# Optimization experiments

Hardware: AMD Instinct MI355X
Metric: run time of the kernel (lower is better)

Reference implementation:

```python
import jax, jax.numpy as jnp
import numpy as np
import math

NH = 12      # num attention heads
WIN = 128    # one-sided sliding window
NG = 32      # number of global (prefix) tokens
NEG = -1e9
LN_EPS = 1e-12


def _layernorm(x, g, b):
    mu = jnp.mean(x, axis=-1, keepdims=True)
    var = jnp.mean(jnp.square(x - mu), axis=-1, keepdims=True)
    return (x - mu) * jax.lax.rsqrt(var + LN_EPS) * g + b


def _longformer_self_attn(h, am, Wq, bq, Wk, bk, Wv, bv):
    B, S, D = h.shape
    Dh = D // NH
    w = WIN
    C = S // w  # number of chunks

    def proj(Wm, bm):
        return (h @ Wm + bm).reshape(B, S, NH, Dh).transpose(0, 2, 1, 3)

    q = proj(Wq, bq) * (1.0 / math.sqrt(Dh))  # [B,H,S,Dh]
    k = proj(Wk, bk)
    v = proj(Wv, bv)

    # ---- banded (sliding window) scores, chunked: each query chunk sees 3w keys ----
    kp = jnp.pad(k, ((0, 0), (0, 0), (w, w), (0, 0)))
    vp = jnp.pad(v, ((0, 0), (0, 0), (w, w), (0, 0)))
    idx = jnp.arange(C)[:, None] * w + jnp.arange(3 * w)[None, :]  # [C,3w]
    k3 = kp[:, :, idx]  # [B,H,C,3w,Dh]
    v3 = vp[:, :, idx]
    qc = q.reshape(B, NH, C, w, Dh)
    band = jnp.einsum('bhcqd,bhckd->bhcqk', qc, k3)  # [B,H,C,w,3w]

    qpos = (jnp.arange(C) * w)[:, None, None] + jnp.arange(w)[None, :, None]  # [C,w,1]
    kpos = (idx - w)[:, None, :]  # [C,1,3w] absolute key positions
    valid = (jnp.abs(kpos - qpos) <= w) & (kpos >= NG) & (kpos < S)  # band, exclude global keys

    amp = jnp.pad(am, ((0, 0), (w, w)))
    am3 = amp[:, idx]  # [B,C,3w] additive mask gathered per chunk
    band = band + am3[:, None, :, None, :]
    band = jnp.where(valid[None, None], band, NEG)
    band = band.reshape(B, NH, S, 3 * w)

    # ---- every token also attends to the NG global tokens ----
    gsc = jnp.einsum('bhsd,bhgd->bhsg', q, k[:, :, :NG]) + am[:, None, None, :NG]

    logits = jnp.concatenate([band, gsc], axis=-1)  # [B,H,S,3w+NG]
    probs = jax.nn.softmax(logits, axis=-1)
    pb = probs[..., :3 * w].reshape(B, NH, C, w, 3 * w)
    out = jnp.einsum('bhcqk,bhckd->bhcqd', pb, v3).reshape(B, NH, S, Dh)
    out = out + jnp.einsum('bhsg,bhgd->bhsd', probs[..., 3 * w:], v[:, :, :NG])

    # ---- global tokens attend to everything ----
    gl = jnp.einsum('bhgd,bhsd->bhgs', q[:, :, :NG], k) + am[:, None, None, :]
    outg = jnp.einsum('bhgs,bhsd->bhgd', jax.nn.softmax(gl, axis=-1), v)

    ctx = jnp.concatenate([outg, out[:, :, NG:]], axis=2)  # [B,H,S,Dh]
    return ctx.transpose(0, 2, 1, 3).reshape(B, S, D)


def setup_inputs() -> dict:
    key = jax.random.key(0)
    ks = jax.random.split(key, 8)
    B, S, D, F = 2, 4096, 768, 3072
    p = lambda k_, sh: jax.random.normal(k_, sh, jnp.float32) * 0.02
    return {
        'hidden_states': jax.random.normal(ks[0], (B, S, D), jnp.float32),
        'attention_mask': jnp.zeros((B, S), jnp.float32),
        'Wq': p(ks[1], (D, D)), 'bq': jnp.zeros((D,), jnp.float32),
        'Wk': p(ks[2], (D, D)), 'bk': jnp.zeros((D,), jnp.float32),
        'Wv': p(ks[3], (D, D)), 'bv': jnp.zeros((D,), jnp.float32),
        'Wo': p(ks[4], (D, D)), 'bo': jnp.zeros((D,), jnp.float32),
        'ln1_g': jnp.ones((D,), jnp.float32), 'ln1_b': jnp.zeros((D,), jnp.float32),
        'Wi': p(ks[5], (D, F)), 'bi': jnp.zeros((F,), jnp.float32),
        'Wo2': p(ks[6], (F, D)), 'bo2': jnp.zeros((D,), jnp.float32),
        'ln2_g': jnp.ones((D,), jnp.float32), 'ln2_b': jnp.zeros((D,), jnp.float32),
    }


def reference(hidden_states, attention_mask, Wq, bq, Wk, bk, Wv, bv, Wo, bo,
              ln1_g, ln1_b, Wi, bi, Wo2, bo2, ln2_g, ln2_b):
    ctx = _longformer_self_attn(hidden_states, attention_mask, Wq, bq, Wk, bk, Wv, bv)
    attn_out = _layernorm(ctx @ Wo + bo + hidden_states, ln1_g, ln1_b)
    inter = jax.nn.gelu(attn_out @ Wi + bi, approximate=False)
    layer_out = _layernorm(inter @ Wo2 + bo2 + attn_out, ln2_g, ln2_b)
    return layer_out
```

## Files before the change

kernel.cpp:

```cpp
#include <hip/hip_runtime.h>
#include <math.h>

#define NHEAD 12
#define DH 64
#define S_LEN 4096
#define B_SZ 2
#define D_MODEL 768
#define FF_DIM 3072
#define WINSZ 128
#define NGLB 32
#define NEGV -1e9f
#define NQC 6291456L

typedef __attribute__((ext_vector_type(8))) short bf16x8;
typedef __attribute__((ext_vector_type(4))) float floatx4;

__device__ __forceinline__ unsigned short f2bf(float x) {
    union { float f; unsigned u; } v; v.f = x;
    unsigned r = v.u + 0x7fffu + ((v.u >> 16) & 1u);
    return (unsigned short)(r >> 16);
}
__device__ __forceinline__ float bf2f(unsigned short x) {
    union { unsigned u; float f; } v; v.u = ((unsigned)x) << 16;
    return v.f;
}

__device__ __forceinline__ void async_copy16(const unsigned short* g, unsigned short* l) {
    __builtin_amdgcn_global_load_lds(
        (const __attribute__((address_space(1))) void*)g,
        (__attribute__((address_space(3))) void*)l, 16, 0, 0);
}

__global__ __launch_bounds__(256) void conv_k(
    const float* __restrict__ x, unsigned short* __restrict__ y, long n)
{
    long i = ((long)blockIdx.x * 256 + threadIdx.x) * 4;
    if (i >= n) return;
    float4 v = *(const float4*)(x + i);
    ushort4 o;
    o.x = f2bf(v.x); o.y = f2bf(v.y); o.z = f2bf(v.z); o.w = f2bf(v.w);
    *(ushort4*)(y + i) = o;
}

__global__ __launch_bounds__(256) void bcat_k(
    const float* __restrict__ a, const float* __restrict__ b,
    const float* __restrict__ c, float* __restrict__ o)
{
    int i = blockIdx.x * 256 + threadIdx.x;
    if (i < 768) o[i] = a[i];
    else if (i < 1536) o[i] = b[i - 768];
    else if (i < 2304) o[i] = c[i - 1536];
}

__global__ __launch_bounds__(256) void transpose_k(
    const float* __restrict__ W, unsigned short* __restrict__ WT, int K, int N)
{
    __shared__ float tile[32][33];
    const int tx = threadIdx.x, ty = threadIdx.y;
    const int n0 = blockIdx.x * 32, k0 = blockIdx.y * 32;
#pragma unroll
    for (int i = 0; i < 4; ++i)
        tile[ty + 8 * i][tx] = W[(long)(k0 + ty + 8 * i) * N + n0 + tx];
    __syncthreads();
#pragma unroll
    for (int i = 0; i < 4; ++i)
        WT[(long)(n0 + ty + 8 * i) * K + k0 + tx] = f2bf(tile[tx][ty + 8 * i]);
}

__global__ __launch_bounds__(256) void vt_k(
    const unsigned short* __restrict__ v, unsigned short* __restrict__ vt)
{
    const int bh = blockIdx.y;
    const int s0 = blockIdx.x * 32;
    const int w = threadIdx.x >> 6, lane = threadIdx.x & 63;
    const unsigned short* src = v + ((long)bh * S_LEN + s0 + w * 8) * DH + lane;
    unsigned short r[8];
#pragma unroll
    for (int j = 0; j < 8; ++j) r[j] = src[j * DH];
    unsigned short* dst = vt + ((long)bh * DH + lane) * S_LEN + s0 + w * 8;
    ushort4 lo, hi;
    lo.x = r[0]; lo.y = r[1]; lo.z = r[2]; lo.w = r[3];
    hi.x = r[4]; hi.y = r[5]; hi.z = r[6]; hi.w = r[7];
    *(ushort4*)dst = lo;
    *(ushort4*)(dst + 4) = hi;
}

template <int EPI>
__global__ __launch_bounds__(256) void gemm_bf(
    const unsigned short* __restrict__ A, const unsigned short* __restrict__ BT,
    const float* __restrict__ bias, const float* __restrict__ resid,
    void* __restrict__ out, int M, int N, int K, int nx)
{
    __shared__ unsigned short As[128 * 32];
    __shared__ unsigned short Bs[128 * 32];
    const int tid = threadIdx.x;
    const int wave = tid >> 6, lane = tid & 63;
    const int t8 = (blockIdx.x & 7) * (gridDim.x >> 3) + (blockIdx.x >> 3);
    const int m0 = (t8 / nx) * 128, n0 = (t8 % nx) * 128;
    const int wr = (wave >> 1) * 64, wc = (wave & 1) * 64;

    floatx4 acc[4][4];
#pragma unroll
    for (int i = 0; i < 4; ++i)
#pragma unroll
        for (int j = 0; j < 4; ++j) acc[i][j] = (floatx4){0.f, 0.f, 0.f, 0.f};

    const int srow = lane >> 2;
    const int schk = (lane & 3) * 8;
    const int r = lane & 15;
    const int q8 = (lane >> 4) * 8;

    for (int k0 = 0; k0 < K; k0 += 32) {
#pragma unroll
        for (int gi = 0; gi < 2; ++gi) {
            const int g = wave * 2 + gi;
            async_copy16(A + (long)(m0 + g * 16 + srow) * K + k0 + schk, &As[g * 512]);
            async_copy16(BT + (long)(n0 + g * 16 + srow) * K + k0 + schk, &Bs[g * 512]);
        }
        __syncthreads();

        bf16x8 af[4], bfr[4];
#pragma unroll
        for (int i = 0; i < 4; ++i) {
            af[i]  = *(const bf16x8*)&As[(wr + i * 16 + r) * 32 + q8];
            bfr[i] = *(const bf16x8*)&Bs[(wc + i * 16 + r) * 32 + q8];
        }
#pragma unroll
        for (int i = 0; i < 4; ++i)
#pragma unroll
            for (int j = 0; j < 4; ++j)
                acc[i][j] = __builtin_amdgcn_mfma_f32_16x16x32_bf16(
                    af[i], bfr[j], acc[i][j], 0, 0, 0);
        __syncthreads();
    }

    const int col_l = lane & 15, row_l = (lane >> 4) * 4;
#pragma unroll
    for (int i = 0; i < 4; ++i) {
#pragma unroll
        for (int j = 0; j < 4; ++j) {
            const int n = n0 + wc + j * 16 + col_l;
            const float bv = bias[n];
#pragma unroll
            for (int rg = 0; rg < 4; ++rg) {
                const int m = m0 + wr + i * 16 + row_l + rg;
                float v = acc[i][j][rg] + bv;
                if (EPI == 0) {
                    ((float*)out)[(long)m * N + n] = v + resid[(long)m * N + n];
                } else if (EPI == 1) {
                    v = 0.5f * v * (1.f + erff(v * 0.70710678118654752f));
                    ((unsigned short*)out)[(long)m * N + n] = f2bf(v);
                } else {
                    const int bb = m >> 12, s = m & 4095;
                    const int part = n / 768;
                    const int nn = n - part * 768;
                    const int hh = nn >> 6, dh = nn & 63;
                    const float sc = (part == 0) ? 0.125f : 1.f;
                    ((unsigned short*)out)[(long)part * NQC +
                        (((long)bb * NHEAD + hh) * S_LEN + s) * DH + dh] = f2bf(v * sc);
                }
            }
        }
    }
}

__global__ __launch_bounds__(256) void band_mfma_k(
    const unsigned short* __restrict__ q, const unsigned short* __restrict__ k,
    const unsigned short* __restrict__ vt, const float* __restrict__ am,
    unsigned short* __restrict__ ctx)
{
    __shared__ unsigned short Ks[32 * 72];
    __shared__ unsigned short Vs[64 * 40];
    __shared__ unsigned short Ps[4][32 * 40];

    const int blk = blockIdx.x;
    const int c = blk & 31;
    const int h = (blk >> 5) % NHEAD;
    const int b = blk / (32 * NHEAD);
    const int tid = threadIdx.x;
    const int wave = tid >> 6, lane = tid & 63;
    const long bh = (long)b * NHEAD + h;

    const unsigned short* kh  = k + bh * S_LEN * DH;
    const unsigned short* vth = vt + bh * (long)DH * S_LEN;
    const float* amb = am + (long)b * S_LEN;

    const int q0 = c * WINSZ + wave * 32;
    const int ln15 = lane & 15, ln4 = lane >> 4;

    bf16x8 qf[2][2];
#pragma unroll
    for (int nt = 0; nt < 2; ++nt)
#pragma unroll
        for (int ks = 0; ks < 2; ++ks)
            qf[nt][ks] = *(const bf16x8*)(q + (bh * S_LEN + q0 + nt * 16 + ln15) * DH
                                          + ks * 32 + ln4 * 8);

    floatx4 o[4][2];
#pragma unroll
    for (int mt = 0; mt < 4; ++mt)
#pragma unroll
        for (int nt = 0; nt < 2; ++nt) o[mt][nt] = (floatx4){0.f, 0.f, 0.f, 0.f};
    float m_r[2] = {-1e30f, -1e30f}, l_r[2] = {0.f, 0.f};

    const int sk_key = tid >> 3, sk_ch = tid & 7;
    const int sv_dim = tid & 63, sv_ch = tid >> 6;
    const bf16x8 zero8 = {0, 0, 0, 0, 0, 0, 0, 0};

    for (int tile = 0; tile < 13; ++tile) {
        const bool glob = (tile == 12);
        const int kbase = glob ? 0 : (c * WINSZ - WINSZ + tile * 32);

        __syncthreads();
        {
            int kpos = kbase + sk_key;
            bf16x8 val = zero8;
            if ((unsigned)kpos < (unsigned)S_LEN)
                val = *(const bf16x8*)(kh + (long)kpos * DH + sk_ch * 8);
            *(bf16x8*)(&Ks[sk_key * 72 + sk_ch * 8]) = val;
        }
        {
            int kc = kbase + sv_ch * 8;
            bf16x8 val = zero8;
            if (kc >= 0 && kc + 8 <= S_LEN)
                val = *(const bf16x8*)(vth + (long)sv_dim * S_LEN + kc);
            *(bf16x8*)(&Vs[sv_dim * 40 + sv_ch * 8]) = val;
        }
        __syncthreads();

        bf16x8 ak[2][2];
#pragma unroll
        for (int mt = 0; mt < 2; ++mt)
#pragma unroll
            for (int ks = 0; ks < 2; ++ks)
                ak[mt][ks] = *(const bf16x8*)(&Ks[(mt * 16 + ln15) * 72 + ks * 32 + ln4 * 8]);

        floatx4 s[2][2];
#pragma unroll
        for (int mt = 0; mt < 2; ++mt)
#pragma unroll
            for (int nt = 0; nt < 2; ++nt) {
                floatx4 acc = (floatx4){0.f, 0.f, 0.f, 0.f};
                acc = __builtin_amdgcn_mfma_f32_16x16x32_bf16(ak[mt][0], qf[nt][0], acc, 0, 0, 0);
                acc = __builtin_amdgcn_mfma_f32_16x16x32_bf16(ak[mt][1], qf[nt][1], acc, 0, 0, 0);
                s[mt][nt] = acc;
            }

#pragma unroll
        for (int mt = 0; mt < 2; ++mt) {
            const int kp0 = kbase + mt * 16 + ln4 * 4;
#pragma unroll
            for (int rg = 0; rg < 4; ++rg) {
                const int kpos = kp0 + rg;
                const bool kin = (unsigned)kpos < (unsigned)S_LEN;
                const float amv = kin ? amb[kpos] : 0.f;
#pragma unroll
                for (int nt = 0; nt < 2; ++nt) {
                    const int qpos = q0 + nt * 16 + ln15;
                    const int dlt = kpos > qpos ? kpos - qpos : qpos - kpos;
                    const bool valid = glob || (kpos >= NGLB && kin && dlt <= WINSZ);
                    s[mt][nt][rg] = valid ? s[mt][nt][rg] + amv : NEGV;
                }
            }
        }

        float alpha[2];
#pragma unroll
        for (int nt = 0; nt < 2; ++nt) {
            float mx = s[0][nt][0];
#pragma unroll
            for (int rg = 1; rg < 4; ++rg) mx = fmaxf(mx, s[0][nt][rg]);
#pragma unroll
            for (int rg = 0; rg < 4; ++rg) mx = fmaxf(mx, s[1][nt][rg]);
            mx = fmaxf(mx, __shfl_xor(mx, 16));
            mx = fmaxf(mx, __shfl_xor(mx, 32));
            const float mn = fmaxf(m_r[nt], mx);
            alpha[nt] = __expf(m_r[nt] - mn);
            m_r[nt] = mn;
        }

#pragma unroll
        for (int nt = 0; nt < 2; ++nt) {
            float sum = 0.f;
#pragma unroll
            for (int mt = 0; mt < 2; ++mt) {
                ushort4 pk;
#pragma unroll
                for (int rg = 0; rg < 4; ++rg) {
                    const float p = __expf(s[mt][nt][rg] - m_r[nt]);
                    sum += p;
                    ((unsigned short*)&pk)[rg] = f2bf(p);
                }
                *(ushort4*)(&Ps[wave][(nt * 16 + ln15) * 40 + mt * 16 + ln4 * 4]) = pk;
            }
            sum += __shfl_xor(sum, 16);
            sum += __shfl_xor(sum, 32);
            l_r[nt] = l_r[nt] * alpha[nt] + sum;
        }

#pragma unroll
        for (int mt = 0; mt < 4; ++mt)
#pragma unroll
            for (int nt = 0; nt < 2; ++nt)
#pragma unroll
                for (int rg = 0; rg < 4; ++rg) o[mt][nt][rg] *= alpha[nt];

        bf16x8 av[4], bp[2];
#pragma unroll
        for (int mt = 0; mt < 4; ++mt)
            av[mt] = *(const bf16x8*)(&Vs[(mt * 16 + ln15) * 40 + ln4 * 8]);
#pragma unroll
        for (int nt = 0; nt < 2; ++nt)
            bp[nt] = *(const bf16x8*)(&Ps[wave][(nt * 16 + ln15) * 40 + ln4 * 8]);
#pragma unroll
        for (int mt = 0; mt < 4; ++mt)
#pragma unroll
            for (int nt = 0; nt < 2; ++nt)
                o[mt][nt] = __builtin_amdgcn_mfma_f32_16x16x32_bf16(
                    av[mt], bp[nt], o[mt][nt], 0, 0, 0);
    }

    const float inv0 = 1.f / l_r[0], inv1 = 1.f / l_r[1];
#pragma unroll
    for (int nt = 0; nt < 2; ++nt) {
        const float inv = nt ? inv1 : inv0;
        const long row = (long)b * S_LEN + q0 + nt * 16 + ln15;
#pragma unroll
        for (int mt = 0; mt < 4; ++mt) {
            ushort4 ov;
#pragma unroll
            for (int rg = 0; rg < 4; ++rg)
                ((unsigned short*)&ov)[rg] = f2bf(o[mt][nt][rg] * inv);
            *(ushort4*)(ctx + row * D_MODEL + h * DH + mt * 16 + ln4 * 4) = ov;
        }
    }
}

__global__ __launch_bounds__(512) void glob_mfma_k(
    const unsigned short* __restrict__ q, const unsigned short* __restrict__ k,
    const unsigned short* __restrict__ vt, const float* __restrict__ am,
    unsigned short* __restrict__ ctx)
{
    __shared__ unsigned short Ps[8][32 * 72];
    __shared__ float Om[64 * 36];
    __shared__ float mW[8][32], lW[8][32], lTot[32];

    const int bh = blockIdx.x;
    const int b = bh / NHEAD, h = bh % NHEAD;
    const int tid = threadIdx.x;
    const int wave = tid >> 6, lane = tid & 63;
    const int ln15 = lane & 15, ln4 = lane >> 4;

    const unsigned short* kh  = k + (long)bh * S_LEN * DH;
    const unsigned short* vth = vt + (long)bh * DH * S_LEN;
    const float* amb = am + (long)b * S_LEN;

    bf16x8 qf[2][2];
#pragma unroll
    for (int nt = 0; nt < 2; ++nt)
#pragma unroll
        for (int ks = 0; ks < 2; ++ks)
            qf[nt][ks] = *(const bf16x8*)(q + ((long)bh * S_LEN + nt * 16 + ln15) * DH
                                          + ks * 32 + ln4 * 8);

    floatx4 o[4][2];
#pragma unroll
    for (int mt = 0; mt < 4; ++mt)
#pragma unroll
        for (int nt = 0; nt < 2; ++nt) o[mt][nt] = (floatx4){0.f, 0.f, 0.f, 0.f};
    float m_r[2] = {-1e30f, -1e30f}, l_r[2] = {0.f, 0.f};

    for (int it = 0; it < 8; ++it) {
        const int kbase = it * 512 + wave * 64;

        bf16x8 ak[4][2];
#pragma unroll
        for (int mt = 0; mt < 4; ++mt)
#pragma unroll
            for (int ks = 0; ks < 2; ++ks)
                ak[mt][ks] = *(const bf16x8*)(kh + (long)(kbase + mt * 16 + ln15) * DH
                                              + ks * 32 + ln4 * 8);

        floatx4 s[4][2];
#pragma unroll
        for (int mt = 0; mt < 4; ++mt)
#pragma unroll
            for (int nt = 0; nt < 2; ++nt) {
                floatx4 acc = (floatx4){0.f, 0.f, 0.f, 0.f};
                acc = __builtin_amdgcn_mfma_f32_16x16x32_bf16(ak[mt][0], qf[nt][0], acc, 0, 0, 0);
                acc = __builtin_amdgcn_mfma_f32_16x16x32_bf16(ak[mt][1], qf[nt][1], acc, 0, 0, 0);
                s[mt][nt] = acc;
            }

#pragma unroll
        for (int mt = 0; mt < 4; ++mt) {
            const int kp0 = kbase + mt * 16 + ln4 * 4;
#pragma unroll
            for (int rg = 0; rg < 4; ++rg) {
                const float amv = amb[kp0 + rg];
#pragma unroll
                for (int nt = 0; nt < 2; ++nt) s[mt][nt][rg] += amv;
            }
        }

        float alpha[2];
#pragma unroll
        for (int nt = 0; nt < 2; ++nt) {
            float mx = s[0][nt][0];
#pragma unroll
            for (int mt = 0; mt < 4; ++mt)
#pragma unroll
                for (int rg = 0; rg < 4; ++rg) mx = fmaxf(mx, s[mt][nt][rg]);
            mx = fmaxf(mx, __shfl_xor(mx, 16));
            mx = fmaxf(mx, __shfl_xor(mx, 32));
            const float mn = fmaxf(m_r[nt], mx);
            alpha[nt] = __expf(m_r[nt] - mn);
            m_r[nt] = mn;
        }

#pragma unroll
        for (int nt = 0; nt < 2; ++nt) {
            float sum = 0.f;
#pragma unroll
            for (int mt = 0; mt < 4; ++mt) {
                ushort4 pk;
#pragma unroll
                for (int rg = 0; rg < 4; ++rg) {
                    const float p = __expf(s[mt][nt][rg] - m_r[nt]);
                    sum += p;
                    ((unsigned short*)&pk)[rg] = f2bf(p);
                }
                *(ushort4*)(&Ps[wave][(nt * 16 + ln15) * 72 + mt * 16 + ln4 * 4]) = pk;
            }
            sum += __shfl_xor(sum, 16);
            sum += __shfl_xor(sum, 32);
            l_r[nt] = l_r[nt] * alpha[nt] + sum;
        }

#pragma unroll
        for (int mt = 0; mt < 4; ++mt)
#pragma unroll
            for (int nt = 0; nt < 2; ++nt)
#pragma unroll
                for (int rg = 0; rg < 4; ++rg) o[mt][nt][rg] *= alpha[nt];

        bf16x8 av[4][2], bp[2][2];
#pragma unroll
        for (int mt = 0; mt < 4; ++mt)
#pragma unroll
            for (int ks = 0; ks < 2; ++ks)
                av[mt][ks] = *(const bf16x8*)(vth + (long)(mt * 16 + ln15) * S_LEN
                                              + kbase + ks * 32 + ln4 * 8);
#pragma unroll
        for (int nt = 0; nt < 2; ++nt)
#pragma unroll
            for (int ks = 0; ks < 2; ++ks)
                bp[nt][ks] = *(const bf16x8*)(&Ps[wave][(nt * 16 + ln15) * 72
                                              + ks * 32 + ln4 * 8]);
#pragma unroll
        for (int mt = 0; mt < 4; ++mt)
#pragma unroll
            for (int nt = 0; nt < 2; ++nt) {
                o[mt][nt] = __builtin_amdgcn_mfma_f32_16x16x32_bf16(
                    av[mt][0], bp[nt][0], o[mt][nt], 0, 0, 0);
                o[mt][nt] = __builtin_amdgcn_mfma_f32_16x16x32_bf16(
                    av[mt][1], bp[nt][1], o[mt][nt], 0, 0, 0);
            }
    }

    if (ln4 == 0) {
#pragma unroll
        for (int nt = 0; nt < 2; ++nt) {
            mW[wave][nt * 16 + ln15] = m_r[nt];
            lW[wave][nt * 16 + ln15] = l_r[nt];
        }
    }
    for (int i = tid; i < 64 * 36; i += 512) Om[i] = 0.f;
    __syncthreads();

    float f[2];
#pragma unroll
    for (int nt = 0; nt < 2; ++nt) {
        const int qq = nt * 16 + ln15;
        float mt_ = mW[0][qq];
#pragma unroll
        for (int w = 1; w < 8; ++w) mt_ = fmaxf(mt_, mW[w][qq]);
        float lt = 0.f;
#pragma unroll
        for (int w = 0; w < 8; ++w) lt += __expf(mW[w][qq] - mt_) * lW[w][qq];
        f[nt] = __expf(m_r[nt] - mt_);
        if (wave == 0 && ln4 == 0) lTot[qq] = lt;
    }
#pragma unroll
    for (int mt = 0; mt < 4; ++mt)
#pragma unroll
        for (int nt = 0; nt < 2; ++nt)
#pragma unroll
            for (int rg = 0; rg < 4; ++rg) o[mt][nt][rg] *= f[nt];

    for (int wv = 0; wv < 8; ++wv) {
        if (wave == wv) {
#pragma unroll
            for (int mt = 0; mt < 4; ++mt)
#pragma unroll
                for (int nt = 0; nt < 2; ++nt)
#pragma unroll
                    for (int rg = 0; rg < 4; ++rg)
                        Om[(mt * 16 + ln4 * 4 + rg) * 36 + nt * 16 + ln15] += o[mt][nt][rg];
        }
        __syncthreads();
    }

    const int qq = tid >> 4, d0 = (tid & 15) * 4;
    const float inv = 1.f / lTot[qq];
    ushort4 ov;
#pragma unroll
    for (int i = 0; i < 4; ++i)
        ((unsigned short*)&ov)[i] = f2bf(Om[(d0 + i) * 36 + qq] * inv);
    *(ushort4*)(ctx + ((long)b * S_LEN + qq) * D_MODEL + h * DH + d0) = ov;
}

__global__ __launch_bounds__(256) void ln_k(
    const float* __restrict__ in, float* __restrict__ out,
    unsigned short* __restrict__ out_bf,
    const float* __restrict__ gw, const float* __restrict__ bw)
{
    __shared__ float red[256];
    const long row = blockIdx.x;
    const float* x = in + row * D_MODEL;
    const int t = threadIdx.x;
    float v0 = x[t], v1 = x[t + 256], v2 = x[t + 512];

    red[t] = v0 + v1 + v2;
    __syncthreads();
    for (int off = 128; off; off >>= 1) {
        if (t < off) red[t] += red[t + off];
        __syncthreads();
    }
    const float mu = red[0] * (1.f / 768.f);
    __syncthreads();

    float d0 = v0 - mu, d1 = v1 - mu, d2 = v2 - mu;
    red[t] = d0 * d0 + d1 * d1 + d2 * d2;
    __syncthreads();
    for (int off = 128; off; off >>= 1) {
        if (t < off) red[t] += red[t + off];
        __syncthreads();
    }
    const float var = red[0] * (1.f / 768.f);
    const float rs = rsqrtf(var + 1e-12f);

    const float y0 = d0 * rs * gw[t] + bw[t];
    const float y1 = d1 * rs * gw[t + 256] + bw[t + 256];
    const float y2 = d2 * rs * gw[t + 512] + bw[t + 512];
    float* y = out + row * D_MODEL;
    y[t] = y0; y[t + 256] = y1; y[t + 512] = y2;
    if (out_bf) {
        unsigned short* yb = out_bf + row * D_MODEL;
        yb[t] = f2bf(y0); yb[t + 256] = f2bf(y1); yb[t + 512] = f2bf(y2);
    }
}

extern "C" void kernel_launch(void* const* d_in, const int* in_sizes, int n_in,
                              void* d_out, int out_size, void* d_ws, size_t ws_size,
                              hipStream_t stream)
{
    const float* hid  = (const float*)d_in[0];
    const float* am   = (const float*)d_in[1];
    const float* Wq   = (const float*)d_in[2];
    const float* bq   = (const float*)d_in[3];
    const float* Wk   = (const float*)d_in[4];
    const float* bk   = (const float*)d_in[5];
    const float* Wv   = (const float*)d_in[6];
    const float* bv   = (const float*)d_in[7];
    const float* Wo   = (const float*)d_in[8];
    const float* bo   = (const float*)d_in[9];
    const float* ln1g = (const float*)d_in[10];
    const float* ln1b = (const float*)d_in[11];
    const float* Wi   = (const float*)d_in[12];
    const float* bi   = (const float*)d_in[13];
    const float* Wo2  = (const float*)d_in[14];
    const float* bo2  = (const float*)d_in[15];
    const float* ln2g = (const float*)d_in[16];
    const float* ln2b = (const float*)d_in[17];

    const long M  = (long)B_SZ * S_LEN;
    const long NQ = NQC;

    unsigned short* W16 = (unsigned short*)d_ws;
    unsigned short* qb   = W16;
    unsigned short* kb   = W16 + NQ;
    unsigned short* vb   = W16 + 2 * NQ;
    unsigned short* vtb  = W16 + 3 * NQ;
    unsigned short* ctxb = W16 + 4 * NQ;
    unsigned short* hidb = W16 + 5 * NQ;
    unsigned short* wqt  = W16 + 6 * NQ;
    unsigned short* wkt  = wqt + 589824;
    unsigned short* wvt  = wkt + 589824;
    unsigned short* wot  = wvt + 589824;
    unsigned short* wit  = wot + 589824;
    unsigned short* wo2t = wit + 2359296;
    float* tmp = (float*)(W16 + 44826624);
    float* bcat = (float*)(W16 + 57409536);
    unsigned short* interb = W16;
    unsigned short* attnb  = hidb;
    float* tmp2 = (float*)(W16 + 4 * NQ);
    (void)ws_size; (void)in_sizes; (void)n_in; (void)out_size;

    transpose_k<<<dim3(24, 24), dim3(32, 8), 0, stream>>>(Wq, wqt, 768, 768);
    transpose_k<<<dim3(24, 24), dim3(32, 8), 0, stream>>>(Wk, wkt, 768, 768);
    transpose_k<<<dim3(24, 24), dim3(32, 8), 0, stream>>>(Wv, wvt, 768, 768);
    transpose_k<<<dim3(24, 24), dim3(32, 8), 0, stream>>>(Wo, wot, 768, 768);
    transpose_k<<<dim3(96, 24), dim3(32, 8), 0, stream>>>(Wi, wit, 768, 3072);
    transpose_k<<<dim3(24, 96), dim3(32, 8), 0, stream>>>(Wo2, wo2t, 3072, 768);
    conv_k<<<dim3((NQ / 4 + 255) / 256), dim3(256), 0, stream>>>(hid, hidb, NQ);
    bcat_k<<<dim3(9), dim3(256), 0, stream>>>(bq, bk, bv, bcat);

    dim3 blk(256);

    gemm_bf<2><<<dim3(1152), blk, 0, stream>>>(hidb, wqt, bcat, nullptr, qb,
                                               M, 2304, 768, 18);

    vt_k<<<dim3(128, 24), blk, 0, stream>>>(vb, vtb);

    band_mfma_k<<<dim3(768), blk, 0, stream>>>(qb, kb, vtb, am, ctxb);
    glob_mfma_k<<<dim3(B_SZ * NHEAD), dim3(512), 0, stream>>>(qb, kb, vtb, am, ctxb);

    gemm_bf<0><<<dim3(384), blk, 0, stream>>>(ctxb, wot, bo, hid, tmp,
                                              M, 768, 768, 6);
    ln_k<<<dim3(M), blk, 0, stream>>>(tmp, tmp, attnb, ln1g, ln1b);

    gemm_bf<1><<<dim3(1536), blk, 0, stream>>>(attnb, wit, bi, nullptr, interb,
                                               M, 3072, 768, 24);

    gemm_bf<0><<<dim3(384), blk, 0, stream>>>(interb, wo2t, bo2, tmp, tmp2,
                                              M, 768, 3072, 6);
    ln_k<<<dim3(M), blk, 0, stream>>>(tmp2, (float*)d_out, nullptr, ln2g, ln2b);
}
```

Baseline: 473.8 us.

## Split-K the N=768 GEMMs and fuse partial sum, bias, residual into layernorm

The two output-projection GEMMs with N=768 only launched 384 tiles, so they are split into two K halves (768 blocks), each writing fp32 partials. The layernorm kernel now sums the two partials, adds bias and residual, and normalizes, which removes the residual epilogue from the GEMM. The shared-memory chunk index is also XOR-swizzled in all GEMMs to reduce LDS bank conflicts. The cost is extra fp32 partial writes and reads.

```diff
diff --git a/kernel.cpp b/kernel.cpp
--- a/kernel.cpp
+++ b/kernel.cpp
@@ -88,8 +88,8 @@
 template <int EPI>
 __global__ __launch_bounds__(256) void gemm_bf(
     const unsigned short* __restrict__ A, const unsigned short* __restrict__ BT,
-    const float* __restrict__ bias, const float* __restrict__ resid,
-    void* __restrict__ out, int M, int N, int K, int nx)
+    const float* __restrict__ bias, void* __restrict__ out,
+    int M, int N, int K, int nx)
 {
     __shared__ unsigned short As[128 * 32];
     __shared__ unsigned short Bs[128 * 32];
@@ -106,9 +106,9 @@
         for (int j = 0; j < 4; ++j) acc[i][j] = (floatx4){0.f, 0.f, 0.f, 0.f};
 
     const int srow = lane >> 2;
-    const int schk = (lane & 3) * 8;
+    const int schk = (((lane & 3) ^ (srow & 3))) * 8;
     const int r = lane & 15;
-    const int q8 = (lane >> 4) * 8;
+    const int q8 = ((lane >> 4) ^ (lane & 3)) * 8;
 
     for (int k0 = 0; k0 < K; k0 += 32) {
 #pragma unroll
@@ -145,9 +145,7 @@
             for (int rg = 0; rg < 4; ++rg) {
                 const int m = m0 + wr + i * 16 + row_l + rg;
                 float v = acc[i][j][rg] + bv;
-                if (EPI == 0) {
-                    ((float*)out)[(long)m * N + n] = v + resid[(long)m * N + n];
-                } else if (EPI == 1) {
+                if (EPI == 1) {
                     v = 0.5f * v * (1.f + erff(v * 0.70710678118654752f));
                     ((unsigned short*)out)[(long)m * N + n] = f2bf(v);
                 } else {
@@ -164,6 +162,73 @@
     }
 }
 
+__global__ __launch_bounds__(256) void gemm_sp(
+    const unsigned short* __restrict__ A, const unsigned short* __restrict__ BT,
+    float* __restrict__ p0, float* __restrict__ p1,
+    int M, int N, int K2, int nx, int ntile)
+{
+    __shared__ unsigned short As[128 * 32];
+    __shared__ unsigned short Bs[128 * 32];
+    const int tid = threadIdx.x;
+    const int wave = tid >> 6, lane = tid & 63;
+    const int t8 = (blockIdx.x & 7) * (gridDim.x >> 3) + (blockIdx.x >> 3);
+    const int slice = t8 >= ntile;
+    const int tile = t8 - slice * ntile;
+    const int m0 = (tile / nx) * 128, n0 = (tile % nx) * 128;
+    const int kbeg = slice * K2, kend = kbeg + K2;
+    float* P = slice ? p1 : p0;
+    const int wr = (wave >> 1) * 64, wc = (wave & 1) * 64;
+
+    floatx4 acc[4][4];
+#pragma unroll
+    for (int i = 0; i < 4; ++i)
+#pragma unroll
+        for (int j = 0; j < 4; ++j) acc[i][j] = (floatx4){0.f, 0.f, 0.f, 0.f};
+
+    const int srow = lane >> 2;
+    const int schk = (((lane & 3) ^ (srow & 3))) * 8;
+    const int r = lane & 15;
+    const int q8 = ((lane >> 4) ^ (lane & 3)) * 8;
+    const long Kl = (long)K2 * 2;
+
+    for (int k0 = kbeg; k0 < kend; k0 += 32) {
+#pragma unroll
+        for (int gi = 0; gi < 2; ++gi) {
+            const int g = wave * 2 + gi;
+            async_copy16(A + (long)(m0 + g * 16 + srow) * Kl + k0 + schk, &As[g * 512]);
+            async_copy16(BT + (long)(n0 + g * 16 + srow) * Kl + k0 + schk, &Bs[g * 512]);
+        }
+        __syncthreads();
+
+        bf16x8 af[4], bfr[4];
+#pragma unroll
+        for (int i = 0; i < 4; ++i) {
+            af[i]  = *(const bf16x8*)&As[(wr + i * 16 + r) * 32 + q8];
+            bfr[i] = *(const bf16x8*)&Bs[(wc + i * 16 + r) * 32 + q8];
+        }
+#pragma unroll
+        for (int i = 0; i < 4; ++i)
+#pragma unroll
+            for (int j = 0; j < 4; ++j)
+                acc[i][j] = __builtin_amdgcn_mfma_f32_16x16x32_bf16(
+                    af[i], bfr[j], acc[i][j], 0, 0, 0);
+        __syncthreads();
+    }
+
+    const int col_l = lane & 15, row_l = (lane >> 4) * 4;
+#pragma unroll
+    for (int i = 0; i < 4; ++i)
+#pragma unroll
+        for (int j = 0; j < 4; ++j) {
+            const int n = n0 + wc + j * 16 + col_l;
+#pragma unroll
+            for (int rg = 0; rg < 4; ++rg) {
+                const int m = m0 + wr + i * 16 + row_l + rg;
+                P[(long)m * N + n] = acc[i][j][rg];
+            }
+        }
+}
+
 __global__ __launch_bounds__(256) void band_mfma_k(
     const unsigned short* __restrict__ q, const unsigned short* __restrict__ k,
     const unsigned short* __restrict__ vt, const float* __restrict__ am,
@@ -520,16 +585,19 @@
     *(ushort4*)(ctx + ((long)b * S_LEN + qq) * D_MODEL + h * DH + d0) = ov;
 }
 
-__global__ __launch_bounds__(256) void ln_k(
-    const float* __restrict__ in, float* __restrict__ out,
-    unsigned short* __restrict__ out_bf,
+__global__ __launch_bounds__(256) void ln2p_k(
+    const float* __restrict__ p0, const float* __restrict__ p1,
+    const float* __restrict__ bias, const float* __restrict__ resid,
+    float* __restrict__ out, unsigned short* __restrict__ out_bf,
     const float* __restrict__ gw, const float* __restrict__ bw)
 {
     __shared__ float red[256];
     const long row = blockIdx.x;
-    const float* x = in + row * D_MODEL;
+    const long base = row * D_MODEL;
     const int t = threadIdx.x;
-    float v0 = x[t], v1 = x[t + 256], v2 = x[t + 512];
+    float v0 = p0[base + t]       + p1[base + t]       + bias[t]       + resid[base + t];
+    float v1 = p0[base + t + 256] + p1[base + t + 256] + bias[t + 256] + resid[base + t + 256];
+    float v2 = p0[base + t + 512] + p1[base + t + 512] + bias[t + 512] + resid[base + t + 512];
 
     red[t] = v0 + v1 + v2;
     __syncthreads();
@@ -553,10 +621,12 @@
     const float y0 = d0 * rs * gw[t] + bw[t];
     const float y1 = d1 * rs * gw[t + 256] + bw[t + 256];
     const float y2 = d2 * rs * gw[t + 512] + bw[t + 512];
-    float* y = out + row * D_MODEL;
-    y[t] = y0; y[t + 256] = y1; y[t + 512] = y2;
+    if (out) {
+        float* y = out + base;
+        y[t] = y0; y[t + 256] = y1; y[t + 512] = y2;
+    }
     if (out_bf) {
-        unsigned short* yb = out_bf + row * D_MODEL;
+        unsigned short* yb = out_bf + base;
         yb[t] = f2bf(y0); yb[t + 256] = f2bf(y1); yb[t + 512] = f2bf(y2);
     }
 }
@@ -600,11 +670,14 @@
     unsigned short* wot  = wvt + 589824;
     unsigned short* wit  = wot + 589824;
     unsigned short* wo2t = wit + 2359296;
-    float* tmp = (float*)(W16 + 44826624);
-    float* bcat = (float*)(W16 + 57409536);
+    float* tmp   = (float*)(W16 + 44826624);
+    float* partB1 = (float*)(W16 + 57409536);
+    float* bcat  = (float*)(W16 + 69992448);
+    float* partA0 = (float*)W16;
+    float* partA1 = (float*)(W16 + 2 * NQ);
     unsigned short* interb = W16;
     unsigned short* attnb  = hidb;
-    float* tmp2 = (float*)(W16 + 4 * NQ);
+    float* partB0 = (float*)(W16 + 4 * NQ);
     (void)ws_size; (void)in_sizes; (void)n_in; (void)out_size;
 
     transpose_k<<<dim3(24, 24), dim3(32, 8), 0, stream>>>(Wq, wqt, 768, 768);
@@ -618,7 +691,7 @@
 
     dim3 blk(256);
 
-    gemm_bf<2><<<dim3(1152), blk, 0, stream>>>(hidb, wqt, bcat, nullptr, qb,
+    gemm_bf<2><<<dim3(1152), blk, 0, stream>>>(hidb, wqt, bcat, qb,
                                                M, 2304, 768, 18);
 
     vt_k<<<dim3(128, 24), blk, 0, stream>>>(vb, vtb);
@@ -626,14 +699,16 @@
     band_mfma_k<<<dim3(768), blk, 0, stream>>>(qb, kb, vtb, am, ctxb);
     glob_mfma_k<<<dim3(B_SZ * NHEAD), dim3(512), 0, stream>>>(qb, kb, vtb, am, ctxb);
 
-    gemm_bf<0><<<dim3(384), blk, 0, stream>>>(ctxb, wot, bo, hid, tmp,
-                                              M, 768, 768, 6);
-    ln_k<<<dim3(M), blk, 0, stream>>>(tmp, tmp, attnb, ln1g, ln1b);
-
-    gemm_bf<1><<<dim3(1536), blk, 0, stream>>>(attnb, wit, bi, nullptr, interb,
+    gemm_sp<<<dim3(768), blk, 0, stream>>>(ctxb, wot, partA0, partA1,
+                                           M, 768, 384, 6, 384);
+    ln2p_k<<<dim3(M), blk, 0, stream>>>(partA0, partA1, bo, hid,
+                                        tmp, attnb, ln1g, ln1b);
+
+    gemm_bf<1><<<dim3(1536), blk, 0, stream>>>(attnb, wit, bi, interb,
                                                M, 3072, 768, 24);
 
-    gemm_bf<0><<<dim3(384), blk, 0, stream>>>(interb, wo2t, bo2, tmp, tmp2,
-                                              M, 768, 3072, 6);
-    ln_k<<<dim3(M), blk, 0, stream>>>(tmp2, (float*)d_out, nullptr, ln2g, ln2b);
-}
+    gemm_sp<<<dim3(768), blk, 0, stream>>>(interb, wo2t, partB0, partB1,
+                                           M, 768, 1536, 6, 384);
+    ln2p_k<<<dim3(M), blk, 0, stream>>>(partB0, partB1, bo2, tmp,
+                                        (float*)d_out, nullptr, ln2g, ln2b);
+}
```

New measurement: 459.0 us. 3.1% less time.
